# Optimization experiments

Measured on AMD Instinct MI355X. Metric: run time of the kernel, lower is better.

## Reference

```python
import jax, jax.numpy as jnp
import numpy as np

N = 262144   # active voxels
C = 128      # channels (in == out)
B, Z, Y, X = 2, 41, 512, 512
EPS = 1e-3   # BN eps from norm_cfg


def _build_neighbors():
    """Build submanifold rulebook-style neighbor tables along z, y, x axes.
    Each table is [N, 3] (offsets -1, 0, +1); missing neighbor -> sentinel N
    (points at a zero-padded feature row)."""
    rng = np.random.default_rng(0)
    total = B * Z * Y * X
    lin = np.sort(rng.choice(total, size=N, replace=False)).astype(np.int64)
    lookup = np.full(total, -1, dtype=np.int64)
    lookup[lin] = np.arange(N)
    r = lin % (Z * Y * X)
    z = r // (Y * X)
    r2 = r % (Y * X)
    y = r2 // X
    x = r2 % X

    def nbrs(axis_vals, axis_size, stride):
        cols = []
        for off in (-1, 0, 1):
            v = axis_vals + off
            valid = (v >= 0) & (v < axis_size)
            nlin = np.clip(lin + off * stride, 0, total - 1)
            idx = np.where(valid, lookup[nlin], -1)
            idx = np.where(idx < 0, N, idx)
            cols.append(idx)
        return np.stack(cols, axis=1).astype(np.int32)

    return nbrs(z, Z, Y * X), nbrs(y, Y, X), nbrs(x, X, 1)


def setup_inputs() -> dict:
    key = jax.random.key(0)
    ks = jax.random.split(key, 8)
    nbr_z, nbr_y, nbr_x = _build_neighbors()
    scale = 1.0 / np.sqrt(3 * C)
    inp = {
        "features": jax.random.normal(ks[0], (N, C), dtype=jnp.float32),
        "W1": jax.random.normal(ks[1], (3, C, C), dtype=jnp.float32) * scale,  # conv3x1x1
        "W2": jax.random.normal(ks[2], (3, C, C), dtype=jnp.float32) * scale,  # conv1x3x1
        "W3": jax.random.normal(ks[3], (3, C, C), dtype=jnp.float32) * scale,  # conv1x1x3
        "g0": jax.random.normal(ks[4], (C,), dtype=jnp.float32) * 0.1 + 1.0,
        "b0": jnp.zeros((C,), dtype=jnp.float32),
        "m0": jax.random.normal(ks[5], (C,), dtype=jnp.float32) * 0.1,
        "v0": jax.random.uniform(ks[5], (C,), minval=0.5, maxval=1.5, dtype=jnp.float32),
        "g2": jax.random.normal(ks[6], (C,), dtype=jnp.float32) * 0.1 + 1.0,
        "b2": jnp.zeros((C,), dtype=jnp.float32),
        "m2": jax.random.normal(ks[6], (C,), dtype=jnp.float32) * 0.1,
        "v2": jax.random.uniform(ks[6], (C,), minval=0.5, maxval=1.5, dtype=jnp.float32),
        "g3": jax.random.normal(ks[7], (C,), dtype=jnp.float32) * 0.1 + 1.0,
        "b3": jnp.zeros((C,), dtype=jnp.float32),
        "m3": jax.random.normal(ks[7], (C,), dtype=jnp.float32) * 0.1,
        "v3": jax.random.uniform(ks[7], (C,), minval=0.5, maxval=1.5, dtype=jnp.float32),
        "nbr_z": jnp.asarray(nbr_z),
        "nbr_y": jnp.asarray(nbr_y),
        "nbr_x": jnp.asarray(nbr_x),
    }
    return inp


def _subm_conv(feats, nbr, W):
    # submanifold gather-matmul: out[n] = sum_k W[k] @ feats[nbr[n,k]] (sentinel -> 0)
    feats_pad = jnp.concatenate([feats, jnp.zeros((1, feats.shape[1]), feats.dtype)], axis=0)
    gathered = feats_pad[nbr]  # [N, 3, C]
    return jnp.einsum('nkc,kcd->nd', gathered, W)


def _bn(x, g, b, m, v):
    return (x - m) * (g * jax.lax.rsqrt(v + EPS)) + b


def reference(features, W1, W2, W3, g0, b0, m0, v0, g2, b2, m2, v2,
              g3, b3, m3, v3, nbr_z, nbr_y, nbr_x):
    # Branch 1: conv3x1x1 -> bn0 -> sigmoid, then (source bug) bn0_2 -> sigmoid applied again
    s = jax.nn.sigmoid(_bn(_subm_conv(features, nbr_z, W1), g0, b0, m0, v0))
    s = jax.nn.sigmoid(_bn(s, g2, b2, m2, v2))
    # Branch 2: conv1x3x1, added raw (its BN/act were mistakenly applied to branch 1)
    s2 = _subm_conv(features, nbr_y, W2)
    # Branch 3: conv1x1x3 -> bn0_3 -> sigmoid
    s3 = jax.nn.sigmoid(_bn(_subm_conv(features, nbr_x, W3), g3, b3, m3, v3))
    return (s + s2 + s3) * features
```

## Files before the change

kernel.cpp:

```cpp
#include <hip/hip_runtime.h>
#include <hip/hip_bf16.h>
#include <stdint.h>
#include <stddef.h>

#define NVOX 262144
#define CCH 128
#define BN_EPS 1e-3f

typedef __attribute__((ext_vector_type(8))) short bfrag;
typedef __attribute__((ext_vector_type(4))) float f4;

#define AS1 __attribute__((address_space(1)))
#define AS3 __attribute__((address_space(3)))

__device__ __forceinline__ unsigned short f2bf(float f) {
  union { float f; unsigned u; } v; v.f = f;
  unsigned r = v.u + 0x7fffu + ((v.u >> 16) & 1u);
  return (unsigned short)(r >> 16);
}

__device__ __forceinline__ bfrag pack8(f4 x, f4 y) {
  bfrag r;
  r[0] = (short)f2bf(x[0]); r[1] = (short)f2bf(x[1]);
  r[2] = (short)f2bf(x[2]); r[3] = (short)f2bf(x[3]);
  r[4] = (short)f2bf(y[0]); r[5] = (short)f2bf(y[1]);
  r[6] = (short)f2bf(y[2]); r[7] = (short)f2bf(y[3]);
  return r;
}

__device__ __forceinline__ float sigmoidf_(float x) {
  return 1.f / (1.f + __expf(-x));
}

__device__ __forceinline__ float bf2f(unsigned short h) {
  union { unsigned u; float f; } v; v.u = ((unsigned)h) << 16; return v.f;
}

__global__ void prep_wfrag(const float* __restrict__ W1, const float* __restrict__ W2,
                           const float* __restrict__ W3, unsigned short* __restrict__ wf) {
  const int frag = blockIdx.x;
  const int tile = frag & 7;
  const int kc   = (frag >> 3) & 3;
  const int tap  = (frag >> 5) % 3;
  const int conv = frag / 96;
  const float* W = (conv == 0) ? W1 : ((conv == 1) ? W2 : W3);
  const int l   = threadIdx.x;
  const int col = tile * 16 + (l & 15);
  const int k0  = kc * 32 + (l >> 4) * 8;
  bfrag o;
#pragma unroll
  for (int e = 0; e < 8; ++e)
    o[e] = (short)f2bf(W[(size_t)(tap * CCH + k0 + e) * CCH + col]);
  *reinterpret_cast<bfrag*>(wf + (size_t)frag * 512 + l * 8) = o;
}

__global__ void prep_bn(const float* g0, const float* b0, const float* m0, const float* v0,
                        const float* g2, const float* b2, const float* m2, const float* v2,
                        const float* g3, const float* b3, const float* m3, const float* v3,
                        float* __restrict__ bn) {
  const int c = threadIdx.x;
  const float s0 = g0[c] * rsqrtf(v0[c] + BN_EPS);
  const float s2 = g2[c] * rsqrtf(v2[c] + BN_EPS);
  const float s3 = g3[c] * rsqrtf(v3[c] + BN_EPS);
  bn[0 * CCH + c] = s0; bn[1 * CCH + c] = b0[c] - m0[c] * s0;
  bn[2 * CCH + c] = s2; bn[3 * CCH + c] = b2[c] - m2[c] * s2;
  bn[4 * CCH + c] = s3; bn[5 * CCH + c] = b3[c] - m3[c] * s3;
}

__global__ void prep_bf16(const float* __restrict__ feats, unsigned short* __restrict__ fbf) {
  const size_t base = ((size_t)blockIdx.x * 256 + threadIdx.x) * 8;
  const f4 x = *reinterpret_cast<const f4*>(feats + base);
  const f4 y = *reinterpret_cast<const f4*>(feats + base + 4);
  *reinterpret_cast<bfrag*>(fbf + base) = pack8(x, y);
  if (blockIdx.x == 0 && threadIdx.x < 16) {
    bfrag z = {0, 0, 0, 0, 0, 0, 0, 0};
    *reinterpret_cast<bfrag*>(fbf + (size_t)NVOX * CCH + threadIdx.x * 8) = z;
  }
}

__global__ __launch_bounds__(1024, 4)
void recon_v7(const unsigned short* __restrict__ fbf,
              const unsigned short* __restrict__ wfrag,
              const float* __restrict__ bn,
              const int* __restrict__ nbrz, const int* __restrict__ nbrx,
              const int* __restrict__ nbry,
              float* __restrict__ out) {
  __shared__ unsigned short Bb[73728];

  const int tid  = threadIdx.x;
  const int lane = tid & 63;
  const int w    = tid >> 6;
  const int l15  = lane & 15;
  const int lhi  = lane >> 4;
  const int cb   = blockIdx.x & 1;
  const int row0 = (blockIdx.x >> 1) * 256;
  const int wrow = row0 + w * 16;

#pragma unroll
  for (int i = 0; i < 9; ++i) {
    const int r = (i < 3) ? i : ((i < 6) ? i + 3 : i - 3);
    const int g = (r * 4 + (w >> 2)) * 8 + cb * 4 + (w & 3);
    __builtin_amdgcn_global_load_lds(
        (const AS1 void*)(wfrag + (size_t)g * 512 + lane * 8),
        (AS3 void*)((char*)Bb + (i * 16 + w) * 1024), 16, 0, 0);
  }
  const int row = wrow + l15;
  const int rg  = row * 3;
  const int izp = nbrz[rg + 0], izn = nbrz[rg + 2];
  const int ixp = nbrx[rg + 0], ixn = nbrx[rg + 2];
  const int iyp = nbry[rg + 0], iyn = nbry[rg + 2];

  asm volatile("s_waitcnt vmcnt(0)" ::: "memory");
  __syncthreads();

  f4 acc[4], run[4];
#pragma unroll
  for (int ct = 0; ct < 4; ++ct) {
    acc[ct] = f4{0.f, 0.f, 0.f, 0.f};
    run[ct] = f4{0.f, 0.f, 0.f, 0.f};
  }

  bfrag aF[4];
  bfrag aS[4];

  const bool azp = __any(izp != NVOX), azn = __any(izn != NVOX);
  const bool axp = __any(ixp != NVOX), axn = __any(ixn != NVOX);
  const bool ayp = __any(iyp != NVOX), ayn = __any(iyn != NVOX);

#define LOADF(DST, IDX) {                                                     \
    const char* p = (const char*)fbf + ((size_t)(unsigned)(IDX) << 8) + (lhi << 4); \
    DST[0] = *reinterpret_cast<const bfrag*>(p);                              \
    DST[1] = *reinterpret_cast<const bfrag*>(p + 64);                         \
    DST[2] = *reinterpret_cast<const bfrag*>(p + 128);                        \
    DST[3] = *reinterpret_cast<const bfrag*>(p + 192);                        \
  }

#define TAP(SLOT, AFR, ACCS) {                                                \
    const char* bs = (const char*)Bb + (SLOT) * 16384 + lane * 16;            \
    _Pragma("unroll")                                                         \
    for (int kc = 0; kc < 4; ++kc) {                                          \
      _Pragma("unroll")                                                       \
      for (int ct = 0; ct < 4; ++ct) {                                        \
        const bfrag b = *reinterpret_cast<const bfrag*>(                      \
            bs + (kc * 4 + ct) * 1024);                                       \
        ACCS[ct] = __builtin_amdgcn_mfma_f32_16x16x32_bf16(                   \
            AFR[kc], b, ACCS[ct], 0, 0, 0);                                   \
      } } }

  LOADF(aS, row)

  if (azp) { LOADF(aF, izp)  TAP(0, aF, acc) }
  TAP(1, aS, acc)
  if (azn) { LOADF(aF, izn)  TAP(2, aF, acc) }
#pragma unroll
  for (int ct = 0; ct < 4; ++ct) {
    const int col = cb * 64 + ct * 16 + l15;
    const float sc0 = bn[0 * CCH + col], sh0 = bn[1 * CCH + col];
    const float sc2 = bn[2 * CCH + col], sh2 = bn[3 * CCH + col];
#pragma unroll
    for (int j = 0; j < 4; ++j) {
      const float u = sigmoidf_(sc0 * acc[ct][j] + sh0);
      run[ct][j] = sigmoidf_(sc2 * u + sh2);
    }
    acc[ct] = f4{0.f, 0.f, 0.f, 0.f};
  }
  if (axp) { LOADF(aF, ixp)  TAP(3, aF, acc) }
  TAP(4, aS, acc)
  if (axn) { LOADF(aF, ixn)  TAP(5, aF, acc) }
#pragma unroll
  for (int ct = 0; ct < 4; ++ct) {
    const int col = cb * 64 + ct * 16 + l15;
    const float sc3 = bn[4 * CCH + col], sh3 = bn[5 * CCH + col];
#pragma unroll
    for (int j = 0; j < 4; ++j)
      run[ct][j] += sigmoidf_(sc3 * acc[ct][j] + sh3);
  }
  if (ayp) { LOADF(aF, iyp)  TAP(6, aF, run) }
  TAP(7, aS, run)
  if (ayn) { LOADF(aF, iyn)  TAP(8, aF, run) }

#undef TAP
#undef LOADF

#pragma unroll
  for (int ct = 0; ct < 4; ++ct) {
    const int col = cb * 64 + ct * 16 + l15;
#pragma unroll
    for (int j = 0; j < 4; ++j) {
      const int r = wrow + (lhi << 2) + j;
      const size_t o = ((size_t)r << 7) + col;
      out[o] = run[ct][j] * bf2f(fbf[o]);
    }
  }
}

__global__ void recon_naive(const float* __restrict__ feats,
    const float* __restrict__ W1, const float* __restrict__ W2, const float* __restrict__ W3,
    const int* __restrict__ nbrz, const int* __restrict__ nbry, const int* __restrict__ nbrx,
    const float* g0, const float* b0, const float* m0, const float* v0,
    const float* g2, const float* b2, const float* m2, const float* v2,
    const float* g3, const float* b3, const float* m3, const float* v3,
    float* __restrict__ out) {
  __shared__ float rows[3][CCH];
  const int n = blockIdx.x;
  const int d = threadIdx.x;
  float res[3];
#pragma unroll
  for (int conv = 0; conv < 3; ++conv) {
    const int* nbr  = (conv == 0) ? nbrz : ((conv == 1) ? nbry : nbrx);
    const float* W  = (conv == 0) ? W1 : ((conv == 1) ? W2 : W3);
#pragma unroll
    for (int tap = 0; tap < 3; ++tap) {
      const int idx = nbr[n * 3 + tap];
      rows[tap][d] = ((unsigned)idx < (unsigned)NVOX) ? feats[((size_t)idx << 7) + d] : 0.f;
    }
    __syncthreads();
    const float* rflat = &rows[0][0];
    float s = 0.f;
    for (int k = 0; k < 3 * CCH; ++k) s += rflat[k] * W[(size_t)k * CCH + d];
    res[conv] = s;
    __syncthreads();
  }
  const float sc0 = g0[d] * rsqrtf(v0[d] + BN_EPS), sh0 = b0[d] - m0[d] * sc0;
  const float sc2 = g2[d] * rsqrtf(v2[d] + BN_EPS), sh2 = b2[d] - m2[d] * sc2;
  const float sc3 = g3[d] * rsqrtf(v3[d] + BN_EPS), sh3 = b3[d] - m3[d] * sc3;
  float u = sigmoidf_(sc0 * res[0] + sh0);
  u = sigmoidf_(sc2 * u + sh2);
  const float s3v = sigmoidf_(sc3 * res[2] + sh3);
  out[((size_t)n << 7) + d] = (u + res[1] + s3v) * feats[((size_t)n << 7) + d];
}

extern "C" void kernel_launch(void* const* d_in, const int* in_sizes, int n_in,
                              void* d_out, int out_size, void* d_ws, size_t ws_size,
                              hipStream_t stream) {
  const float* feats = (const float*)d_in[0];
  const float* W1 = (const float*)d_in[1];
  const float* W2 = (const float*)d_in[2];
  const float* W3 = (const float*)d_in[3];
  const float* g0 = (const float*)d_in[4];
  const float* b0 = (const float*)d_in[5];
  const float* m0 = (const float*)d_in[6];
  const float* v0 = (const float*)d_in[7];
  const float* g2 = (const float*)d_in[8];
  const float* b2 = (const float*)d_in[9];
  const float* m2 = (const float*)d_in[10];
  const float* v2 = (const float*)d_in[11];
  const float* g3 = (const float*)d_in[12];
  const float* b3 = (const float*)d_in[13];
  const float* m3 = (const float*)d_in[14];
  const float* v3 = (const float*)d_in[15];
  const int* nz = (const int*)d_in[16];
  const int* ny = (const int*)d_in[17];
  const int* nx = (const int*)d_in[18];
  float* out = (float*)d_out;

  const size_t wf_bytes = 288u * 1024u;
  const size_t bn_bytes = 4096u;
  const size_t fb_bytes = ((size_t)NVOX + 1) * CCH * sizeof(short);
  if (ws_size >= wf_bytes + bn_bytes + fb_bytes) {
    unsigned short* wf  = (unsigned short*)d_ws;
    float*          bnt = (float*)((char*)d_ws + wf_bytes);
    unsigned short* fbf = (unsigned short*)((char*)d_ws + wf_bytes + bn_bytes);
    hipLaunchKernelGGL(prep_wfrag, dim3(288), dim3(64), 0, stream, W1, W2, W3, wf);
    hipLaunchKernelGGL(prep_bn, dim3(1), dim3(CCH), 0, stream,
                       g0, b0, m0, v0, g2, b2, m2, v2, g3, b3, m3, v3, bnt);
    hipLaunchKernelGGL(prep_bf16, dim3((NVOX * CCH) / (256 * 8)), dim3(256), 0, stream,
                       feats, fbf);
    hipLaunchKernelGGL(recon_v7, dim3((NVOX / 256) * 2), dim3(1024), 0, stream,
                       fbf, wf, bnt, nz, nx, ny, out);
  } else {
    hipLaunchKernelGGL(recon_naive, dim3(NVOX), dim3(CCH), 0, stream,
                       feats, W1, W2, W3, nz, ny, nx,
                       g0, b0, m0, v0, g2, b2, m2, v2, g3, b3, m3, v3, out);
  }
}
```

Measured before the change: 157.1 us.

## Fuse fp32-to-bf16 feature conversion into the main gather-MFMA kernel

Drops the separate prep_bf16 pass that wrote a bf16 copy of all features. The main kernel now gathers fp32 neighbor rows directly and converts them to bf16 fragments in registers, masking missing neighbors by multiplying with zero. It also reorders the loads so the next neighbor's fp32 load is issued before the center tap's MFMAs, overlapping memory with compute. The cost is twice the bytes per gathered row and more registers for the fp32 staging buffers, and the final multiply now uses exact fp32 features.

Result: slower. 188.3 us (+19.9%).

```diff
diff --git a/kernel.cpp b/kernel.cpp
--- a/kernel.cpp
+++ b/kernel.cpp
@@ -30,10 +30,6 @@
 
 __device__ __forceinline__ float sigmoidf_(float x) {
   return 1.f / (1.f + __expf(-x));
-}
-
-__device__ __forceinline__ float bf2f(unsigned short h) {
-  union { unsigned u; float f; } v; v.u = ((unsigned)h) << 16; return v.f;
 }
 
 __global__ void prep_wfrag(const float* __restrict__ W1, const float* __restrict__ W2,
@@ -67,19 +63,8 @@
   bn[4 * CCH + c] = s3; bn[5 * CCH + c] = b3[c] - m3[c] * s3;
 }
 
-__global__ void prep_bf16(const float* __restrict__ feats, unsigned short* __restrict__ fbf) {
-  const size_t base = ((size_t)blockIdx.x * 256 + threadIdx.x) * 8;
-  const f4 x = *reinterpret_cast<const f4*>(feats + base);
-  const f4 y = *reinterpret_cast<const f4*>(feats + base + 4);
-  *reinterpret_cast<bfrag*>(fbf + base) = pack8(x, y);
-  if (blockIdx.x == 0 && threadIdx.x < 16) {
-    bfrag z = {0, 0, 0, 0, 0, 0, 0, 0};
-    *reinterpret_cast<bfrag*>(fbf + (size_t)NVOX * CCH + threadIdx.x * 8) = z;
-  }
-}
-
 __global__ __launch_bounds__(1024, 4)
-void recon_v7(const unsigned short* __restrict__ fbf,
+void recon_v9(const float* __restrict__ feats,
               const unsigned short* __restrict__ wfrag,
               const float* __restrict__ bn,
               const int* __restrict__ nbrz, const int* __restrict__ nbrx,
@@ -110,30 +95,39 @@
   const int ixp = nbrx[rg + 0], ixn = nbrx[rg + 2];
   const int iyp = nbry[rg + 0], iyn = nbry[rg + 2];
 
-  asm volatile("s_waitcnt vmcnt(0)" ::: "memory");
-  __syncthreads();
-
-  f4 acc[4], run[4];
-#pragma unroll
-  for (int ct = 0; ct < 4; ++ct) {
-    acc[ct] = f4{0.f, 0.f, 0.f, 0.f};
-    run[ct] = f4{0.f, 0.f, 0.f, 0.f};
-  }
-
-  bfrag aF[4];
-  bfrag aS[4];
-
   const bool azp = __any(izp != NVOX), azn = __any(izn != NVOX);
   const bool axp = __any(ixp != NVOX), axn = __any(ixn != NVOX);
   const bool ayp = __any(iyp != NVOX), ayn = __any(iyn != NVOX);
-
-#define LOADF(DST, IDX) {                                                     \
-    const char* p = (const char*)fbf + ((size_t)(unsigned)(IDX) << 8) + (lhi << 4); \
-    DST[0] = *reinterpret_cast<const bfrag*>(p);                              \
-    DST[1] = *reinterpret_cast<const bfrag*>(p + 64);                         \
-    DST[2] = *reinterpret_cast<const bfrag*>(p + 128);                        \
-    DST[3] = *reinterpret_cast<const bfrag*>(p + 192);                        \
-  }
+  const int   czp = (izp == NVOX) ? 0 : izp;  const float mzp = (izp == NVOX) ? 0.f : 1.f;
+  const int   czn = (izn == NVOX) ? 0 : izn;  const float mzn = (izn == NVOX) ? 0.f : 1.f;
+  const int   cxp = (ixp == NVOX) ? 0 : ixp;  const float mxp = (ixp == NVOX) ? 0.f : 1.f;
+  const int   cxn = (ixn == NVOX) ? 0 : ixn;  const float mxn = (ixn == NVOX) ? 0.f : 1.f;
+  const int   cyp = (iyp == NVOX) ? 0 : iyp;  const float myp = (iyp == NVOX) ? 0.f : 1.f;
+  const int   cyn = (iyn == NVOX) ? 0 : iyn;  const float myn = (iyn == NVOX) ? 0.f : 1.f;
+
+  f4 fst[8];
+  bfrag aF[4];
+  bfrag aS[4];
+
+#define LOADR(IDX) {                                                          \
+    const float* p = feats + ((size_t)(unsigned)(IDX) << 7) + (lhi << 3);     \
+    fst[0] = *reinterpret_cast<const f4*>(p);                                 \
+    fst[1] = *reinterpret_cast<const f4*>(p + 4);                             \
+    fst[2] = *reinterpret_cast<const f4*>(p + 32);                            \
+    fst[3] = *reinterpret_cast<const f4*>(p + 36);                            \
+    fst[4] = *reinterpret_cast<const f4*>(p + 64);                            \
+    fst[5] = *reinterpret_cast<const f4*>(p + 68);                            \
+    fst[6] = *reinterpret_cast<const f4*>(p + 96);                            \
+    fst[7] = *reinterpret_cast<const f4*>(p + 100);                           \
+  }
+
+#define CVT(DST, ZM) {                                                        \
+    _Pragma("unroll")                                                         \
+    for (int kc = 0; kc < 4; ++kc) {                                          \
+      f4 x = fst[kc * 2] * (ZM);                                              \
+      f4 y = fst[kc * 2 + 1] * (ZM);                                          \
+      DST[kc] = pack8(x, y);                                                  \
+    } }
 
 #define TAP(SLOT, AFR, ACCS) {                                                \
     const char* bs = (const char*)Bb + (SLOT) * 16384 + lane * 16;            \
@@ -147,11 +141,33 @@
             AFR[kc], b, ACCS[ct], 0, 0, 0);                                   \
       } } }
 
-  LOADF(aS, row)
-
-  if (azp) { LOADF(aF, izp)  TAP(0, aF, acc) }
-  TAP(1, aS, acc)
-  if (azn) { LOADF(aF, izn)  TAP(2, aF, acc) }
+#define CONV(VP, VN, CP, MP, CN, MN, SP, SS, SN, ACCS)                        \
+  {                                                                           \
+    if (VP)      LOADR(CP)                                                    \
+    else if (VN) LOADR(CN)                                                    \
+    TAP(SS, aS, ACCS)                                                         \
+    if (VP) {                                                                 \
+      CVT(aF, MP)  TAP(SP, aF, ACCS)                                          \
+      if (VN) { LOADR(CN)  CVT(aF, MN)  TAP(SN, aF, ACCS) }                   \
+    } else if (VN) {                                                          \
+      CVT(aF, MN)  TAP(SN, aF, ACCS)                                          \
+    }                                                                         \
+  }
+
+  LOADR(row)
+  CVT(aS, 1.f)
+
+  asm volatile("s_waitcnt vmcnt(0)" ::: "memory");
+  __syncthreads();
+
+  f4 acc[4], run[4];
+#pragma unroll
+  for (int ct = 0; ct < 4; ++ct) {
+    acc[ct] = f4{0.f, 0.f, 0.f, 0.f};
+    run[ct] = f4{0.f, 0.f, 0.f, 0.f};
+  }
+
+  CONV(azp, azn, czp, mzp, czn, mzn, 0, 1, 2, acc)
 #pragma unroll
   for (int ct = 0; ct < 4; ++ct) {
     const int col = cb * 64 + ct * 16 + l15;
@@ -164,9 +180,7 @@
     }
     acc[ct] = f4{0.f, 0.f, 0.f, 0.f};
   }
-  if (axp) { LOADF(aF, ixp)  TAP(3, aF, acc) }
-  TAP(4, aS, acc)
-  if (axn) { LOADF(aF, ixn)  TAP(5, aF, acc) }
+  CONV(axp, axn, cxp, mxp, cxn, mxn, 3, 4, 5, acc)
 #pragma unroll
   for (int ct = 0; ct < 4; ++ct) {
     const int col = cb * 64 + ct * 16 + l15;
@@ -175,12 +189,12 @@
     for (int j = 0; j < 4; ++j)
       run[ct][j] += sigmoidf_(sc3 * acc[ct][j] + sh3);
   }
-  if (ayp) { LOADF(aF, iyp)  TAP(6, aF, run) }
-  TAP(7, aS, run)
-  if (ayn) { LOADF(aF, iyn)  TAP(8, aF, run) }
-
+  CONV(ayp, ayn, cyp, myp, cyn, myn, 6, 7, 8, run)
+
+#undef CONV
 #undef TAP
-#undef LOADF
+#undef CVT
+#undef LOADR
 
 #pragma unroll
   for (int ct = 0; ct < 4; ++ct) {
@@ -189,7 +203,7 @@
     for (int j = 0; j < 4; ++j) {
       const int r = wrow + (lhi << 2) + j;
       const size_t o = ((size_t)r << 7) + col;
-      out[o] = run[ct][j] * bf2f(fbf[o]);
+      out[o] = run[ct][j] * feats[o];
     }
   }
 }
@@ -256,18 +270,14 @@
 
   const size_t wf_bytes = 288u * 1024u;
   const size_t bn_bytes = 4096u;
-  const size_t fb_bytes = ((size_t)NVOX + 1) * CCH * sizeof(short);
-  if (ws_size >= wf_bytes + bn_bytes + fb_bytes) {
+  if (ws_size >= wf_bytes + bn_bytes) {
     unsigned short* wf  = (unsigned short*)d_ws;
     float*          bnt = (float*)((char*)d_ws + wf_bytes);
-    unsigned short* fbf = (unsigned short*)((char*)d_ws + wf_bytes + bn_bytes);
     hipLaunchKernelGGL(prep_wfrag, dim3(288), dim3(64), 0, stream, W1, W2, W3, wf);
     hipLaunchKernelGGL(prep_bn, dim3(1), dim3(CCH), 0, stream,
                        g0, b0, m0, v0, g2, b2, m2, v2, g3, b3, m3, v3, bnt);
-    hipLaunchKernelGGL(prep_bf16, dim3((NVOX * CCH) / (256 * 8)), dim3(256), 0, stream,
-                       feats, fbf);
-    hipLaunchKernelGGL(recon_v7, dim3((NVOX / 256) * 2), dim3(1024), 0, stream,
-                       fbf, wf, bnt, nz, nx, ny, out);
+    hipLaunchKernelGGL(recon_v9, dim3((NVOX / 256) * 2), dim3(1024), 0, stream,
+                       feats, wf, bnt, nz, nx, ny, out);
   } else {
     hipLaunchKernelGGL(recon_naive, dim3(NVOX), dim3(CCH), 0, stream,
                        feats, W1, W2, W3, nz, ny, nx,
```
